# Performance work log

Measured on AMD Instinct MI355X. Metric: run time of the kernel, lower is better.

Reference implementation:

```python
import jax, jax.numpy as jnp
import numpy as np

N_NODES = 50000
N_EDGES = 1600000
D_IN = 128
D_OUT = 32
ALPHA = 0.2  # LeakyReLU negative slope


def setup_inputs() -> dict:
    key = jax.random.key(0)
    k1, k2, k3, k4, k5, k6 = jax.random.split(key, 6)
    gain = float(np.sqrt(2.0))  # relu gain, xavier_normal-style scale
    X = jax.random.normal(k1, (N_NODES, D_IN), dtype=jnp.float32)
    weights = jax.random.normal(k2, (D_IN, D_OUT), dtype=jnp.float32) * (gain * np.sqrt(2.0 / (D_IN + D_OUT)))
    a0 = jax.random.normal(k3, (1, D_OUT), dtype=jnp.float32) * (gain * np.sqrt(2.0 / (1 + D_OUT)))
    a1 = jax.random.normal(k4, (1, D_OUT), dtype=jnp.float32) * (gain * np.sqrt(2.0 / (1 + D_OUT)))
    row_idx = jax.random.randint(k5, (N_EDGES,), 0, N_NODES, dtype=jnp.int32)
    col_idx = jax.random.randint(k6, (N_EDGES,), 0, N_NODES, dtype=jnp.int32)
    return {"X": X, "weights": weights, "a0": a0, "a1": a1,
            "row_idx": row_idx, "col_idx": col_idx}


def _minmax_norm(v):
    vmin = jnp.min(v)
    vmax = jnp.max(v)
    return (v - vmin) / (vmax - vmin)


def reference(X, weights, a0, a1, row_idx, col_idx):
    # X_prime = X @ W  -> [N, D]
    X_prime = X @ weights
    # Per-node partial scores; edge score e(i->j) = a0.X_prime[i] + a1.X_prime[j]
    s0 = jnp.sum(X_prime * a0, axis=-1)  # [N]
    s1 = jnp.sum(X_prime * a1, axis=-1)  # [N]
    att = s0[row_idx] + s1[col_idx]      # [E]
    # leakyrelu -> min-max normalize over all edges -> exp
    att = jax.nn.leaky_relu(att, negative_slope=ALPHA)
    att = jnp.exp(_minmax_norm(att))
    # rows_sum = SpMM(att, ones) = per-destination-row sum of edge weights
    rows_sum = jax.ops.segment_sum(att, row_idx, num_segments=N_NODES)  # [N]
    # h_prime = SpMM(att, X_prime) / rows_sum  (dropout p=0 -> identity)
    h = jax.ops.segment_sum(att[:, None] * X_prime[col_idx], row_idx,
                            num_segments=N_NODES)  # [N, D]
    return h / rows_sum[:, None]
```

## Files before the change

### kernel.cpp

```cpp
#include <hip/hip_runtime.h>
#include <hip/hip_bf16.h>
#include <math.h>

#define N_NODES 50000
#define N_EDGES 1600000
#define D_IN 128
#define D_OUT 32
#define ALPHA 0.2f

#define NB   256
#define RPB  196
#define CAP  8192
#define GST  16
#define PT   16
#define PBK  256
#define EB   (PT * PBK)
#define NEB  ((N_EDGES + EB - 1) / EB)
#define XNPB 32
#define NXB  ((N_NODES + XNPB - 1) / XNPB)
#define XLS  33

__device__ __forceinline__ int enc_f(float x) {
    int i = __float_as_int(x);
    return i >= 0 ? i : (i ^ 0x7fffffff);
}
__device__ __forceinline__ float dec_f(int k) {
    return __int_as_float(k >= 0 ? k : (k ^ 0x7fffffff));
}
__device__ __forceinline__ unsigned short f2bf(float x) {
    __hip_bfloat16 h = __float2bfloat16(x);
    return *(unsigned short*)&h;
}
__device__ __forceinline__ float bf2f(unsigned short u) {
    return __uint_as_float((unsigned)u << 16);
}

__global__ __launch_bounds__(256) void k_gemm(const float* __restrict__ X,
                                              const float* __restrict__ W,
                                              const float* __restrict__ a0,
                                              const float* __restrict__ a1,
                                              unsigned short* __restrict__ Xpb,
                                              float* __restrict__ s0,
                                              float* __restrict__ s1,
                                              int* __restrict__ gcount) {
    __shared__ float4 Wl4[1024];
    __shared__ float4 Xl4[XNPB * XLS];
    const int tid = threadIdx.x;
    if (blockIdx.x == 0) {
        int4* g4 = (int4*)gcount;
#pragma unroll
        for (int i = 0; i < NB * GST / 4 / 256; ++i)
            g4[tid + 256 * i] = make_int4(0, 0, 0, 0);
    }
    const int node0 = blockIdx.x * XNPB;
    {
        const float4* W4 = (const float4*)W;
#pragma unroll
        for (int i = 0; i < 4; ++i) Wl4[tid + 256 * i] = W4[tid + 256 * i];
        const float4* X4 = (const float4*)X + (size_t)node0 * (D_IN / 4);
        const int lim = (min(XNPB, N_NODES - node0)) * (D_IN / 4);
#pragma unroll
        for (int i = 0; i < 4; ++i) {
            const int idx = tid + 256 * i;
            const float4 v = (idx < lim) ? X4[idx]
                                         : make_float4(0.f, 0.f, 0.f, 0.f);
            Xl4[(idx >> 5) * XLS + (idx & 31)] = v;
        }
    }
    __syncthreads();
    const int g = tid >> 3;
    const int l = tid & 7;
    const int node = node0 + g;
    const float4* xr = &Xl4[g * XLS];
    float ax = 0.f, ay = 0.f, az = 0.f, aw = 0.f;
#pragma unroll 4
    for (int kk = 0; kk < D_IN / 4; ++kk) {
        const float4 xv = xr[kk];
        const float4 w0 = Wl4[(4 * kk + 0) * 8 + l];
        const float4 w1 = Wl4[(4 * kk + 1) * 8 + l];
        const float4 w2 = Wl4[(4 * kk + 2) * 8 + l];
        const float4 w3 = Wl4[(4 * kk + 3) * 8 + l];
        ax += xv.x * w0.x + xv.y * w1.x + xv.z * w2.x + xv.w * w3.x;
        ay += xv.x * w0.y + xv.y * w1.y + xv.z * w2.y + xv.w * w3.y;
        az += xv.x * w0.z + xv.y * w1.z + xv.z * w2.z + xv.w * w3.z;
        aw += xv.x * w0.w + xv.y * w1.w + xv.z * w2.w + xv.w * w3.w;
    }
    if (node < N_NODES) {
        uint2 pk;
        pk.x = ((unsigned)f2bf(ay) << 16) | f2bf(ax);
        pk.y = ((unsigned)f2bf(aw) << 16) | f2bf(az);
        ((uint2*)Xpb)[(size_t)node * 8 + l] = pk;
        const float4 av0 = ((const float4*)a0)[l];
        const float4 av1 = ((const float4*)a1)[l];
        float v0 = ax * av0.x + ay * av0.y + az * av0.z + aw * av0.w;
        float v1 = ax * av1.x + ay * av1.y + az * av1.z + aw * av1.w;
#pragma unroll
        for (int m = 4; m >= 1; m >>= 1) {
            v0 += __shfl_xor(v0, m);
            v1 += __shfl_xor(v1, m);
        }
        if (l == 0) { s0[node] = v0; s1[node] = v1; }
    }
}

__global__ __launch_bounds__(256) void k_edge(const int* __restrict__ row,
                                              const int* __restrict__ col,
                                              const float* __restrict__ s0,
                                              const float* __restrict__ s1,
                                              int* __restrict__ gcount,
                                              int2* __restrict__ mm,
                                              uint2* __restrict__ gEdges) {
    __shared__ uint2 rec[EB];
    __shared__ int hist[NB];
    __shared__ int off[NB + 1];
    __shared__ int lcur[NB];
    __shared__ int gbase[NB];
    __shared__ int smn[4], smx[4];
    const int tid = threadIdx.x;
    if (tid < NB) hist[tid] = 0;
    __syncthreads();
    const int base = blockIdx.x * EB;
    unsigned px[PT];
    float    fa[PT];
    int cnt = 0;
    int kmin = 0x7fffffff, kmax = 0x80000000;
    if (base + EB <= N_EDGES) {
#pragma unroll
        for (int i = 0; i < PT / 4; ++i) {
            const int4 r4 = ((const int4*)(row + base))[tid + i * PBK];
            const int4 c4 = ((const int4*)(col + base))[tid + i * PBK];
            const int rr[4] = {r4.x, r4.y, r4.z, r4.w};
            const int cc[4] = {c4.x, c4.y, c4.z, c4.w};
#pragma unroll
            for (int j = 0; j < 4; ++j) {
                const int r = rr[j];
                const int c = cc[j];
                float a = s0[r] + s1[c];
                a = a > 0.f ? a : ALPHA * a;
                const int k = enc_f(a);
                kmin = min(kmin, k);
                kmax = max(kmax, k);
                const unsigned b = (unsigned)r / RPB;
                const unsigned lr = (unsigned)r - b * RPB;
                px[cnt] = (b << 24) | (lr << 16) | (unsigned)c;
                fa[cnt] = a;
                ++cnt;
                atomicAdd(&hist[b], 1);
            }
        }
    } else {
#pragma unroll
        for (int i = 0; i < PT; ++i) {
            const int e = base + i * PBK + tid;
            if (e >= N_EDGES) break;
            const int r = row[e];
            const int c = col[e];
            float a = s0[r] + s1[c];
            a = a > 0.f ? a : ALPHA * a;
            const int k = enc_f(a);
            kmin = min(kmin, k);
            kmax = max(kmax, k);
            const unsigned b = (unsigned)r / RPB;
            const unsigned lr = (unsigned)r - b * RPB;
            px[cnt] = (b << 24) | (lr << 16) | (unsigned)c;
            fa[cnt] = a;
            ++cnt;
            atomicAdd(&hist[b], 1);
        }
    }
    __syncthreads();
    if (tid < NB) {
        const int h = hist[tid];
        gbase[tid] = h > 0 ? atomicAdd(&gcount[tid << 4], h) : 0;
    }
    if (tid == 0) {
        int run = 0;
        for (int i = 0; i < NB; ++i) { off[i] = run; run += hist[i]; }
        off[NB] = run;
    }
    __syncthreads();
    if (tid < NB) lcur[tid] = off[tid];
    __syncthreads();
    for (int j = 0; j < cnt; ++j) {
        const unsigned b = px[j] >> 24;
        const int p = atomicAdd(&lcur[b], 1);
        rec[p] = make_uint2(px[j], (unsigned)__float_as_int(fa[j]));
    }
    __syncthreads();
    const int total = off[NB];
    for (int i = tid; i < total; i += PBK) {
        const uint2 e = rec[i];
        const unsigned b = e.x >> 24;
        const int pos = gbase[b] + (i - off[b]);
        if (pos < CAP) gEdges[(size_t)b * CAP + pos] = e;
    }
#pragma unroll
    for (int m = 32; m >= 1; m >>= 1) {
        kmin = min(kmin, __shfl_xor(kmin, m));
        kmax = max(kmax, __shfl_xor(kmax, m));
    }
    const int wave = tid >> 6;
    if ((tid & 63) == 0) { smn[wave] = kmin; smx[wave] = kmax; }
    __syncthreads();
    if (tid == 0) {
#pragma unroll
        for (int w = 1; w < 4; ++w) {
            kmin = min(kmin, smn[w]);
            kmax = max(kmax, smx[w]);
        }
        mm[blockIdx.x] = make_int2(kmin, kmax);
    }
}

__global__ __launch_bounds__(1024, 1) void k_bucket(const int* __restrict__ gcount,
                                                    const uint2* __restrict__ gEdges,
                                                    const unsigned short* __restrict__ Xpb,
                                                    const int2* __restrict__ mm,
                                                    float* __restrict__ out) {
    __shared__ unsigned short scol[CAP];
    __shared__ float swt[CAP];
    __shared__ int off[RPB + 1];
    __shared__ int cur[RPB];
    __shared__ int rmn[16], rmx[16];
    __shared__ float s_mn, s_inv;
    const int b = blockIdx.x;
    const int t = threadIdx.x;
    const int cnt = min(gcount[b << 4], CAP);
    const uint2* eb = gEdges + (size_t)b * CAP;

    int kmn = 0x7fffffff, kmx = 0x80000000;
    for (int i = t; i < NEB; i += 1024) {
        const int2 v = mm[i];
        kmn = min(kmn, v.x);
        kmx = max(kmx, v.y);
    }
#pragma unroll
    for (int m = 32; m >= 1; m >>= 1) {
        kmn = min(kmn, __shfl_xor(kmn, m));
        kmx = max(kmx, __shfl_xor(kmx, m));
    }
    if ((t & 63) == 0) { rmn[t >> 6] = kmn; rmx[t >> 6] = kmx; }
    if (t < RPB) cur[t] = 0;
    __syncthreads();
    if (t == 0) {
#pragma unroll
        for (int w = 1; w < 16; ++w) {
            kmn = min(kmn, rmn[w]);
            kmx = max(kmx, rmx[w]);
        }
        const float mn = dec_f(kmn);
        const float mx = dec_f(kmx);
        s_mn = mn;
        s_inv = 1.0f / (mx - mn);
    }
    for (int i = t; i < cnt; i += 1024)
        atomicAdd(&cur[(eb[i].x >> 16) & 0xFFu], 1);
    __syncthreads();
    if (t == 0) {
        int run = 0;
#pragma unroll
        for (int r = 0; r < RPB; ++r) { off[r] = run; run += cur[r]; }
        off[RPB] = run;
    }
    __syncthreads();
    if (t < RPB) cur[t] = off[t];
    __syncthreads();
    const float mn = s_mn;
    const float inv = s_inv;
    for (int i = t; i < cnt; i += 1024) {
        const uint2 e = eb[i];
        const int lr = (int)((e.x >> 16) & 0xFFu);
        const int p = atomicAdd(&cur[lr], 1);
        if (p < CAP) {
            scol[p] = (unsigned short)(e.x & 0xFFFFu);
            swt[p] = __expf((__int_as_float(e.y) - mn) * inv);
        }
    }
    __syncthreads();

    const int proc = t >> 4;
    const int d2 = t & 15;
    const unsigned* Xp32 = (const unsigned*)Xpb;
    for (int lr = proc; lr < RPB; lr += 64) {
        const int s = off[lr];
        const int e2 = off[lr + 1];
        float pa0 = 0.f, pa1 = 0.f, pa2 = 0.f, pa3 = 0.f;
        float pb0 = 0.f, pb1 = 0.f, pb2 = 0.f, pb3 = 0.f;
        float w0s = 0.f, w1s = 0.f, w2s = 0.f, w3s = 0.f;
        int i = s;
        for (; i + 3 < e2; i += 4) {
            const int c0 = scol[i];
            const int c1 = scol[i + 1];
            const int c2 = scol[i + 2];
            const int c3 = scol[i + 3];
            const float w0 = swt[i];
            const float w1 = swt[i + 1];
            const float w2 = swt[i + 2];
            const float w3 = swt[i + 3];
            const unsigned u0 = Xp32[(size_t)c0 * 16 + d2];
            const unsigned u1 = Xp32[(size_t)c1 * 16 + d2];
            const unsigned u2 = Xp32[(size_t)c2 * 16 + d2];
            const unsigned u3 = Xp32[(size_t)c3 * 16 + d2];
            pa0 += w0 * bf2f((unsigned short)(u0 & 0xFFFFu));
            pb0 += w0 * bf2f((unsigned short)(u0 >> 16));
            pa1 += w1 * bf2f((unsigned short)(u1 & 0xFFFFu));
            pb1 += w1 * bf2f((unsigned short)(u1 >> 16));
            pa2 += w2 * bf2f((unsigned short)(u2 & 0xFFFFu));
            pb2 += w2 * bf2f((unsigned short)(u2 >> 16));
            pa3 += w3 * bf2f((unsigned short)(u3 & 0xFFFFu));
            pb3 += w3 * bf2f((unsigned short)(u3 >> 16));
            w0s += w0; w1s += w1; w2s += w2; w3s += w3;
        }
        for (; i < e2; ++i) {
            const float w = swt[i];
            const unsigned u = Xp32[(size_t)scol[i] * 16 + d2];
            pa0 += w * bf2f((unsigned short)(u & 0xFFFFu));
            pb0 += w * bf2f((unsigned short)(u >> 16));
            w0s += w;
        }
        const int r = b * RPB + lr;
        if (r < N_NODES) {
            const float ws = w0s + w1s + w2s + w3s;
            float2 o;
            o.x = (pa0 + pa1 + pa2 + pa3) / ws;
            o.y = (pb0 + pb1 + pb2 + pb3) / ws;
            ((float2*)out)[(size_t)r * 16 + d2] = o;
        }
    }
}

extern "C" void kernel_launch(void* const* d_in, const int* in_sizes, int n_in,
                              void* d_out, int out_size, void* d_ws, size_t ws_size,
                              hipStream_t stream) {
    const float* X  = (const float*)d_in[0];
    const float* W  = (const float*)d_in[1];
    const float* a0 = (const float*)d_in[2];
    const float* a1 = (const float*)d_in[3];
    const int* row  = (const int*)d_in[4];
    const int* col  = (const int*)d_in[5];
    float* out = (float*)d_out;

    float* ws = (float*)d_ws;
    int*   gcount = (int*)ws + 64;
    int2*  mm = (int2*)((int*)ws + 64 + NB * GST);
    float* s0 = ws + 64 + NB * GST + 1024;
    float* s1 = s0 + 50048;
    unsigned short* Xpb = (unsigned short*)(s1 + 50048);
    uint2* gEdges = (uint2*)(s1 + 50048 + 800000);

    k_gemm<<<NXB, 256, 0, stream>>>(X, W, a0, a1, Xpb, s0, s1, gcount);
    k_edge<<<NEB, 256, 0, stream>>>(row, col, s0, s1, gcount, mm, gEdges);
    k_bucket<<<NB, 1024, 0, stream>>>(gcount, gEdges, Xpb, mm, out);
}
```

Measured before the change: 144.2 us.

## Parallelize prefix sums with wave scans and process two nodes per thread in projection

Replaces the serial single-thread exclusive scans over 256 bucket histograms (k_edge) and 196 row counts (k_bucket) with wavefront shuffle-up scans combined across waves through shared memory. Separately, the projection kernel now handles 64 nodes per block, so each thread computes two nodes and reuses each loaded W value twice. The scans remove a serial critical path in which one thread walks hundreds of entries while the rest of the block waits. Doubling nodes per block halves the grid and raises register and shared-memory use in the projection kernel, which may reduce occupancy.

```diff
diff --git a/kernel.cpp b/kernel.cpp
--- a/kernel.cpp
+++ b/kernel.cpp
@@ -16,7 +16,7 @@
 #define PBK  256
 #define EB   (PT * PBK)
 #define NEB  ((N_EDGES + EB - 1) / EB)
-#define XNPB 32
+#define XNPB 64
 #define NXB  ((N_NODES + XNPB - 1) / XNPB)
 #define XLS  33
 
@@ -60,7 +60,7 @@
         const float4* X4 = (const float4*)X + (size_t)node0 * (D_IN / 4);
         const int lim = (min(XNPB, N_NODES - node0)) * (D_IN / 4);
 #pragma unroll
-        for (int i = 0; i < 4; ++i) {
+        for (int i = 0; i < 8; ++i) {
             const int idx = tid + 256 * i;
             const float4 v = (idx < lim) ? X4[idx]
                                          : make_float4(0.f, 0.f, 0.f, 0.f);
@@ -70,36 +70,62 @@
     __syncthreads();
     const int g = tid >> 3;
     const int l = tid & 7;
-    const int node = node0 + g;
-    const float4* xr = &Xl4[g * XLS];
-    float ax = 0.f, ay = 0.f, az = 0.f, aw = 0.f;
+    const float4* xr0 = &Xl4[g * XLS];
+    const float4* xr1 = &Xl4[(g + 32) * XLS];
+    float axA = 0.f, ayA = 0.f, azA = 0.f, awA = 0.f;
+    float axB = 0.f, ayB = 0.f, azB = 0.f, awB = 0.f;
 #pragma unroll 4
     for (int kk = 0; kk < D_IN / 4; ++kk) {
-        const float4 xv = xr[kk];
+        const float4 xa = xr0[kk];
+        const float4 xb = xr1[kk];
         const float4 w0 = Wl4[(4 * kk + 0) * 8 + l];
         const float4 w1 = Wl4[(4 * kk + 1) * 8 + l];
         const float4 w2 = Wl4[(4 * kk + 2) * 8 + l];
         const float4 w3 = Wl4[(4 * kk + 3) * 8 + l];
-        ax += xv.x * w0.x + xv.y * w1.x + xv.z * w2.x + xv.w * w3.x;
-        ay += xv.x * w0.y + xv.y * w1.y + xv.z * w2.y + xv.w * w3.y;
-        az += xv.x * w0.z + xv.y * w1.z + xv.z * w2.z + xv.w * w3.z;
-        aw += xv.x * w0.w + xv.y * w1.w + xv.z * w2.w + xv.w * w3.w;
-    }
-    if (node < N_NODES) {
-        uint2 pk;
-        pk.x = ((unsigned)f2bf(ay) << 16) | f2bf(ax);
-        pk.y = ((unsigned)f2bf(aw) << 16) | f2bf(az);
-        ((uint2*)Xpb)[(size_t)node * 8 + l] = pk;
-        const float4 av0 = ((const float4*)a0)[l];
-        const float4 av1 = ((const float4*)a1)[l];
-        float v0 = ax * av0.x + ay * av0.y + az * av0.z + aw * av0.w;
-        float v1 = ax * av1.x + ay * av1.y + az * av1.z + aw * av1.w;
-#pragma unroll
-        for (int m = 4; m >= 1; m >>= 1) {
-            v0 += __shfl_xor(v0, m);
-            v1 += __shfl_xor(v1, m);
-        }
-        if (l == 0) { s0[node] = v0; s1[node] = v1; }
+        axA += xa.x * w0.x + xa.y * w1.x + xa.z * w2.x + xa.w * w3.x;
+        ayA += xa.x * w0.y + xa.y * w1.y + xa.z * w2.y + xa.w * w3.y;
+        azA += xa.x * w0.z + xa.y * w1.z + xa.z * w2.z + xa.w * w3.z;
+        awA += xa.x * w0.w + xa.y * w1.w + xa.z * w2.w + xa.w * w3.w;
+        axB += xb.x * w0.x + xb.y * w1.x + xb.z * w2.x + xb.w * w3.x;
+        ayB += xb.x * w0.y + xb.y * w1.y + xb.z * w2.y + xb.w * w3.y;
+        azB += xb.x * w0.z + xb.y * w1.z + xb.z * w2.z + xb.w * w3.z;
+        awB += xb.x * w0.w + xb.y * w1.w + xb.z * w2.w + xb.w * w3.w;
+    }
+    const float4 av0 = ((const float4*)a0)[l];
+    const float4 av1 = ((const float4*)a1)[l];
+    {
+        const int node = node0 + g;
+        if (node < N_NODES) {
+            uint2 pk;
+            pk.x = ((unsigned)f2bf(ayA) << 16) | f2bf(axA);
+            pk.y = ((unsigned)f2bf(awA) << 16) | f2bf(azA);
+            ((uint2*)Xpb)[(size_t)node * 8 + l] = pk;
+            float v0 = axA * av0.x + ayA * av0.y + azA * av0.z + awA * av0.w;
+            float v1 = axA * av1.x + ayA * av1.y + azA * av1.z + awA * av1.w;
+#pragma unroll
+            for (int m = 4; m >= 1; m >>= 1) {
+                v0 += __shfl_xor(v0, m);
+                v1 += __shfl_xor(v1, m);
+            }
+            if (l == 0) { s0[node] = v0; s1[node] = v1; }
+        }
+    }
+    {
+        const int node = node0 + g + 32;
+        if (node < N_NODES) {
+            uint2 pk;
+            pk.x = ((unsigned)f2bf(ayB) << 16) | f2bf(axB);
+            pk.y = ((unsigned)f2bf(awB) << 16) | f2bf(azB);
+            ((uint2*)Xpb)[(size_t)node * 8 + l] = pk;
+            float v0 = axB * av0.x + ayB * av0.y + azB * av0.z + awB * av0.w;
+            float v1 = axB * av1.x + ayB * av1.y + azB * av1.z + awB * av1.w;
+#pragma unroll
+            for (int m = 4; m >= 1; m >>= 1) {
+                v0 += __shfl_xor(v0, m);
+                v1 += __shfl_xor(v1, m);
+            }
+            if (l == 0) { s0[node] = v0; s1[node] = v1; }
+        }
     }
 }
 
@@ -115,6 +141,7 @@
     __shared__ int off[NB + 1];
     __shared__ int lcur[NB];
     __shared__ int gbase[NB];
+    __shared__ int wse[4];
     __shared__ int smn[4], smx[4];
     const int tid = threadIdx.x;
     if (tid < NB) hist[tid] = 0;
@@ -169,17 +196,28 @@
         }
     }
     __syncthreads();
-    if (tid < NB) {
-        const int h = hist[tid];
-        gbase[tid] = h > 0 ? atomicAdd(&gcount[tid << 4], h) : 0;
-    }
-    if (tid == 0) {
-        int run = 0;
-        for (int i = 0; i < NB; ++i) { off[i] = run; run += hist[i]; }
-        off[NB] = run;
-    }
-    __syncthreads();
-    if (tid < NB) lcur[tid] = off[tid];
+    const int h = hist[tid];
+    gbase[tid] = h > 0 ? atomicAdd(&gcount[tid << 4], h) : 0;
+    {
+        const int lane = tid & 63;
+        int inc = h;
+#pragma unroll
+        for (int d = 1; d < 64; d <<= 1) {
+            const int u = __shfl_up(inc, d);
+            if (lane >= d) inc += u;
+        }
+        if (lane == 63) wse[tid >> 6] = inc;
+        __syncthreads();
+        int addp = 0;
+        const int wv = tid >> 6;
+#pragma unroll
+        for (int w = 0; w < 4; ++w)
+            if (w < wv) addp += wse[w];
+        const int exc = inc - h + addp;
+        off[tid] = exc;
+        lcur[tid] = exc;
+        if (tid == 255) off[NB] = inc + addp;
+    }
     __syncthreads();
     for (int j = 0; j < cnt; ++j) {
         const unsigned b = px[j] >> 24;
@@ -221,6 +259,7 @@
     __shared__ float swt[CAP];
     __shared__ int off[RPB + 1];
     __shared__ int cur[RPB];
+    __shared__ int wsc[4];
     __shared__ int rmn[16], rmx[16];
     __shared__ float s_mn, s_inv;
     const int b = blockIdx.x;
@@ -256,11 +295,27 @@
     for (int i = t; i < cnt; i += 1024)
         atomicAdd(&cur[(eb[i].x >> 16) & 0xFFu], 1);
     __syncthreads();
-    if (t == 0) {
-        int run = 0;
-#pragma unroll
-        for (int r = 0; r < RPB; ++r) { off[r] = run; run += cur[r]; }
-        off[RPB] = run;
+    int inc_s = 0, v_s = 0;
+    if (t < 256) {
+        v_s = (t < RPB) ? cur[t] : 0;
+        inc_s = v_s;
+        const int lane = t & 63;
+#pragma unroll
+        for (int d = 1; d < 64; d <<= 1) {
+            const int u = __shfl_up(inc_s, d);
+            if (lane >= d) inc_s += u;
+        }
+        if (lane == 63) wsc[t >> 6] = inc_s;
+    }
+    __syncthreads();
+    if (t < 256) {
+        int addp = 0;
+        const int wv = t >> 6;
+#pragma unroll
+        for (int w = 0; w < 4; ++w)
+            if (w < wv) addp += wsc[w];
+        if (t < RPB) off[t] = inc_s - v_s + addp;
+        if (t == 255) off[RPB] = inc_s + addp;
     }
     __syncthreads();
     if (t < RPB) cur[t] = off[t];
```

Measured after the change: 142.5 us. Within noise of the previous version (-1.2%).
